# Optimization experiments

Hardware: AMD Instinct MI355X
Metric: run time of the kernel (lower is better)

Reference implementation:

```python
import jax, jax.numpy as jnp
import numpy as np

B = 128
D_IN = 1024
D_OUT = 512
N_PTS = 8192


def _fps(xyz, npoint):
    """Deterministic farthest_point_sample (initial farthest index = 0).
    xyz: [B, N, 3] -> idx [B, npoint]."""
    Bn, N, _ = xyz.shape
    bidx = jnp.arange(Bn)

    def step(carry, _):
        dist, far = carry
        centroid = xyz[bidx, far]                              # [B, 3]
        d = jnp.sum((xyz - centroid[:, None, :]) ** 2, -1)     # [B, N]
        dist = jnp.minimum(dist, d)
        return (dist, jnp.argmax(dist, -1)), far

    init = (jnp.full((Bn, N), 1e10, xyz.dtype), jnp.zeros((Bn,), jnp.int32))
    _, idxs = jax.lax.scan(step, init, None, length=npoint)    # [npoint, B]
    return idxs.T


def _proj(x, cw, cb, s, t, lw, lb):
    """Conv1d(k=1) -> eval BatchNorm (folded affine) -> ReLU -> Linear over length -> ReLU.
    x: [B, L, D_IN] -> [B, D_OUT, 32]."""
    h = jnp.einsum('bld,od->bol', x, cw) + cb[None, :, None]
    h = jax.nn.relu(h * s[None, :, None] + t[None, :, None])
    return jax.nn.relu(jnp.einsum('bol,sl->bos', h, lw) + lb)


def _pos_enc(xyz, w1, b1, s1, t1, w2, b2, s2, t2):
    """xyz: [B, n, 3] -> [B, n, D_OUT]. Two 1x1 convs with folded-affine BN + ReLU."""
    h = jnp.einsum('bnc,oc->bon', xyz, w1) + b1[None, :, None]
    h = jax.nn.relu(h * s1[None, :, None] + t1[None, :, None])
    h = jnp.einsum('bon,po->bpn', h, w2) + b2[None, :, None]
    h = jax.nn.relu(h * s2[None, :, None] + t2[None, :, None])
    return h.transpose(0, 2, 1)


def setup_inputs() -> dict:
    key = jax.random.key(0)
    ks = iter(jax.random.split(key, 64))

    def rn(shape, scale=0.05):
        return jax.random.normal(next(ks), shape, jnp.float32) * scale

    inp = {
        'rgb_feature': rn((B, 49, D_IN), 1.0),
        'depth_feature': rn((B, 49, D_IN), 1.0),
        'mmwave_feature': rn((B, 32, D_IN), 1.0),
        'lidar_feature': rn((B, 32, D_IN), 1.0),
        'lidar_points': rn((B, N_PTS, 3), 1.0),
    }
    for mod, L in (('rgb', 49), ('depth', 49), ('mmwave', 32), ('lidar', 32)):
        inp[f'{mod}_cw'] = rn((D_OUT, D_IN))
        inp[f'{mod}_cb'] = rn((D_OUT,))
        inp[f'{mod}_bns'] = jax.random.uniform(next(ks), (D_OUT,), jnp.float32, 0.5, 1.5)
        inp[f'{mod}_bnb'] = rn((D_OUT,))
        inp[f'{mod}_lw'] = rn((32, L))
        inp[f'{mod}_lb'] = rn((32,))
    inp['pe_w1'] = rn((128, 3), 0.5)
    inp['pe_b1'] = rn((128,))
    inp['pe_s1'] = jax.random.uniform(next(ks), (128,), jnp.float32, 0.5, 1.5)
    inp['pe_t1'] = rn((128,))
    inp['pe_w2'] = rn((D_OUT, 128))
    inp['pe_b2'] = rn((D_OUT,))
    inp['pe_s2'] = jax.random.uniform(next(ks), (D_OUT,), jnp.float32, 0.5, 1.5)
    inp['pe_t2'] = rn((D_OUT,))
    return inp


def reference(rgb_feature, depth_feature, mmwave_feature, lidar_feature, lidar_points,
              rgb_cw, rgb_cb, rgb_bns, rgb_bnb, rgb_lw, rgb_lb,
              depth_cw, depth_cb, depth_bns, depth_bnb, depth_lw, depth_lb,
              mmwave_cw, mmwave_cb, mmwave_bns, mmwave_bnb, mmwave_lw, mmwave_lb,
              lidar_cw, lidar_cb, lidar_bns, lidar_bnb, lidar_lw, lidar_lb,
              pe_w1, pe_b1, pe_s1, pe_t1, pe_w2, pe_b2, pe_s2, pe_t2):
    feats = [
        _proj(rgb_feature, rgb_cw, rgb_cb, rgb_bns, rgb_bnb, rgb_lw, rgb_lb),
        _proj(depth_feature, depth_cw, depth_cb, depth_bns, depth_bnb, depth_lw, depth_lb),
        _proj(mmwave_feature, mmwave_cw, mmwave_cb, mmwave_bns, mmwave_bnb, mmwave_lw, mmwave_lb),
        _proj(lidar_feature, lidar_cw, lidar_cb, lidar_bns, lidar_bnb, lidar_lw, lidar_lb),
    ]
    projected = jnp.concatenate(feats, axis=2).transpose(0, 2, 1)   # [B, 128, D_OUT]
    npoint = projected.shape[1]
    fps_idx = _fps(lidar_points, npoint)                            # [B, 128]
    new_xyz = jnp.take_along_axis(lidar_points, fps_idx[..., None], axis=1)  # [B, 128, 3]
    pos = _pos_enc(new_xyz, pe_w1, pe_b1, pe_s1, pe_t1, pe_w2, pe_b2, pe_s2, pe_t2)
    return projected + pos
```

## Files before the change

### kernel.cpp

```cpp
#include <hip/hip_runtime.h>
#include <hip/hip_bf16.h>

typedef __attribute__((ext_vector_type(8))) short bf16x8;
typedef __attribute__((ext_vector_type(4))) float f32x4;
typedef __attribute__((ext_vector_type(4))) float vf4;
typedef __attribute__((ext_vector_type(4))) short s16x4;
typedef __attribute__((ext_vector_type(2))) unsigned int u32x2;

__device__ __forceinline__ unsigned short f2bf(float f) {
  __hip_bfloat16 h = __float2bfloat16(f);
  union { __hip_bfloat16 h; unsigned short u; } cv; cv.h = h; return cv.u;
}

__device__ __forceinline__ u32x2 cvt4(vf4 v) {
  union { __hip_bfloat162 h; unsigned u; } a, b;
  a.h = __float22bfloat162_rn(make_float2(v[0], v[1]));
  b.h = __float22bfloat162_rn(make_float2(v[2], v[3]));
  u32x2 r; r[0] = a.u; r[1] = b.u; return r;
}

__device__ __forceinline__ void gemm_tile(const float* __restrict__ A,
                                          const float* __restrict__ W,
                                          const float* __restrict__ cbp,
                                          const float* __restrict__ scp,
                                          const float* __restrict__ shp,
                                          unsigned short* __restrict__ H,
                                          float* __restrict__ out,
                                          const int K, const int nk,
                                          const int mtile, const int ntile,
                                          unsigned short (&As)[128][64],
                                          unsigned short (&Bs)[128][64]) {
  const int t = threadIdx.x, lane = t & 63, wv = t >> 6;
  const int wr = wv >> 2, wc = wv & 3;
  const float* Ap = A + (size_t)(mtile * 128 + (t >> 4)) * K + ((t & 15) << 2);
  const float* Wp = W + (size_t)(ntile * 128 + (t >> 4)) * K + ((t & 15) << 2);
  const int sRow = t >> 4;
  const int sCol = (t & 15) << 2;

  f32x4 acc[4][2];
#pragma unroll
  for (int i = 0; i < 4; ++i)
#pragma unroll
    for (int j = 0; j < 2; ++j) acc[i][j] = (f32x4){0.f, 0.f, 0.f, 0.f};

  for (int ks = 0; ks < nk; ++ks) {
    __syncthreads();
#pragma unroll
    for (int p = 0; p < 4; ++p) {
      const vf4 av  = *(const vf4*)(Ap + (size_t)(p * 32) * K);
      const vf4 wvv = *(const vf4*)(Wp + (size_t)(p * 32) * K);
      *(u32x2*)&As[sRow + p * 32][sCol] = cvt4(av);
      *(u32x2*)&Bs[sRow + p * 32][sCol] = cvt4(wvv);
    }
    __syncthreads();
#pragma unroll
    for (int kk = 0; kk < 2; ++kk) {
      const int kb = (kk << 5) + ((lane >> 4) << 3);
      bf16x8 af[4], bfv[2];
#pragma unroll
      for (int i = 0; i < 4; ++i)
        af[i] = *(const bf16x8*)&As[wr * 64 + i * 16 + (lane & 15)][kb];
#pragma unroll
      for (int j = 0; j < 2; ++j)
        bfv[j] = *(const bf16x8*)&Bs[wc * 32 + j * 16 + (lane & 15)][kb];
#pragma unroll
      for (int i = 0; i < 4; ++i)
#pragma unroll
        for (int j = 0; j < 2; ++j)
          acc[i][j] = __builtin_amdgcn_mfma_f32_16x16x32_bf16(af[i], bfv[j], acc[i][j], 0, 0, 0);
    }
    Ap += 64; Wp += 64;
  }

  const int mbase = mtile * 128 + wr * 64;
  const int nbase = ntile * 128 + wc * 32;
#pragma unroll
  for (int j = 0; j < 2; ++j) {
    const int col = nbase + j * 16 + (lane & 15);
    const float cbv = cbp[col], scv = scp[col], shv = shp[col];
#pragma unroll
    for (int i = 0; i < 4; ++i) {
#pragma unroll
      for (int q = 0; q < 4; ++q) {
        const int row = mbase + i * 16 + ((lane >> 4) << 2) + q;
        float v = acc[i][j][q];
        v = fmaxf(fmaf(v + cbv, scv, shv), 0.f);
        if (H) H[(size_t)row * 512 + col] = f2bf(v);
        else   out[(size_t)row * 512 + col] = v;
      }
    }
  }
}

struct FArgs {
  const float* A[4]; const float* W[4];
  const float* cb[4]; const float* sc[4]; const float* sh[4];
  unsigned short* H[4];
  const float* pts; float* new_xyz;
};

__global__ __launch_bounds__(512) void fused_main(FArgs fa) {
  __shared__ __align__(16) unsigned short As[128][64];
  __shared__ __align__(16) unsigned short Bs[128][64];
  __shared__ unsigned long long red[2][8];
  __shared__ float redC[2][8][3];
  const int bid = blockIdx.x;

  if (bid < 128) {
    const int t = threadIdx.x, wv = t >> 6, lane = t & 63;
    const float* src = fa.pts + (size_t)bid * 8192 * 3;
    float px[16], py[16], pz[16], dist[16];
#pragma unroll
    for (int k = 0; k < 16; ++k) {
      const int p = t + (k << 9);
      px[k] = src[p * 3 + 0]; py[k] = src[p * 3 + 1]; pz[k] = src[p * 3 + 2];
      dist[k] = 1e10f;
    }
    float cx = src[0], cy = src[1], cz = src[2];
    for (int it = 0; it < 128; ++it) {
      if (t == 0) {
        float* o = fa.new_xyz + ((size_t)bid * 128 + it) * 3;
        o[0] = cx; o[1] = cy; o[2] = cz;
      }
      float bd = -1.f, bx = 0.f, by = 0.f, bz = 0.f; int bi = 0;
#pragma unroll
      for (int k = 0; k < 16; ++k) {
        const float dx = px[k] - cx, dy = py[k] - cy, dz = pz[k] - cz;
        const float d = __fadd_rn(__fadd_rn(__fmul_rn(dx, dx), __fmul_rn(dy, dy)),
                                  __fmul_rn(dz, dz));
        const float dk = fminf(dist[k], d);
        dist[k] = dk;
        if (dk > bd) { bd = dk; bi = t + (k << 9); bx = px[k]; by = py[k]; bz = pz[k]; }
      }
      const unsigned long long myKey =
          ((unsigned long long)__float_as_uint(bd) << 13) | (unsigned)(8191 - bi);
      unsigned long long key = myKey;
#pragma unroll
      for (int off = 32; off; off >>= 1) {
        const unsigned long long o = __shfl_xor(key, off);
        key = (o > key) ? o : key;
      }
      const int p = it & 1;
      if (lane == 0) red[p][wv] = key;
      if (myKey == key) {
        redC[p][wv][0] = bx; redC[p][wv][1] = by; redC[p][wv][2] = bz;
      }
      __syncthreads();
      unsigned long long m = red[p][0]; int w = 0;
#pragma unroll
      for (int i = 1; i < 8; ++i) {
        const unsigned long long v = red[p][i];
        if (v > m) { m = v; w = i; }
      }
      cx = redC[p][w][0]; cy = redC[p][w][1]; cz = redC[p][w][2];
    }
  } else {
    const int cb = bid - 128;
    int g, lid;
    if (cb < 196)      { g = 0; lid = cb; }
    else if (cb < 392) { g = 1; lid = cb - 196; }
    else if (cb < 520) { g = 2; lid = cb - 392; }
    else               { g = 3; lid = cb - 520; }
    gemm_tile(fa.A[g], fa.W[g], fa.cb[g], fa.sc[g], fa.sh[g], fa.H[g], nullptr,
              1024, 16, lid >> 2, lid & 3, As, Bs);
  }
}

__global__ __launch_bounds__(256) void posenc_h1(const float* __restrict__ nx,
                                                 const float* __restrict__ w1,
                                                 const float* __restrict__ b1,
                                                 const float* __restrict__ s1,
                                                 const float* __restrict__ t1,
                                                 float* __restrict__ H1) {
  const int gid = blockIdx.x * 256 + threadIdx.x;
  const int row = gid >> 7, j = gid & 127;
  const float x = nx[row * 3 + 0], y = nx[row * 3 + 1], z = nx[row * 3 + 2];
  float v = w1[j * 3 + 0] * x + w1[j * 3 + 1] * y + w1[j * 3 + 2] * z + b1[j];
  v = fmaxf(fmaf(v, s1[j], t1[j]), 0.f);
  H1[gid] = v;
}

struct PArgs {
  const float *A, *W, *cb, *sc, *sh;
  float* out;
};
__global__ __launch_bounds__(512) void gemm_pe(PArgs pa) {
  __shared__ __align__(16) unsigned short As[128][64];
  __shared__ __align__(16) unsigned short Bs[128][64];
  const int lid = blockIdx.x;
  gemm_tile(pa.A, pa.W, pa.cb, pa.sc, pa.sh, nullptr, pa.out,
            128, 2, lid >> 2, lid & 3, As, Bs);
}

struct MArgs {
  const unsigned short *H0, *H1, *H2, *H3;
  const float *lw0, *lw1, *lw2, *lw3;
  const float *lb0, *lb1, *lb2, *lb3;
  float* out;
};

__global__ __launch_bounds__(512) void mix_add(MArgs ma) {
  __shared__ float hs[49 * 512];
  __shared__ float lws[32 * 49];
  __shared__ float lbs[32];
  const int b = blockIdx.x >> 2, mod = blockIdx.x & 3, t = threadIdx.x;
  const unsigned short* H; const float* lw; const float* lb; int L;
  switch (mod) {
    case 0: H = ma.H0; lw = ma.lw0; lb = ma.lb0; L = 49; break;
    case 1: H = ma.H1; lw = ma.lw1; lb = ma.lb1; L = 49; break;
    case 2: H = ma.H2; lw = ma.lw2; lb = ma.lb2; L = 32; break;
    default:H = ma.H3; lw = ma.lw3; lb = ma.lb3; L = 32; break;
  }
  H += (size_t)b * L * 512;
  for (int i = t; i < L * 512; i += 512) hs[i] = __uint_as_float(((unsigned)H[i]) << 16);
  for (int i = t; i < 32 * L; i += 512) lws[i] = lw[i];
  if (t < 32) lbs[t] = lb[t];
  __syncthreads();
  float acc[32];
#pragma unroll
  for (int s = 0; s < 32; ++s) acc[s] = 0.f;
  for (int l = 0; l < L; ++l) {
    const float hv = hs[l * 512 + t];
#pragma unroll
    for (int s = 0; s < 32; ++s) acc[s] = fmaf(hv, lws[s * L + l], acc[s]);
  }
  float* O = ma.out + ((size_t)(b * 128 + mod * 32)) * 512 + t;
#pragma unroll
  for (int s = 0; s < 32; ++s) {
    O[(size_t)s * 512] += fmaxf(acc[s] + lbs[s], 0.f);
  }
}

extern "C" void kernel_launch(void* const* d_in, const int* in_sizes, int n_in,
                              void* d_out, int out_size, void* d_ws, size_t ws_size,
                              hipStream_t stream) {
  const float* rgb    = (const float*)d_in[0];
  const float* depth  = (const float*)d_in[1];
  const float* mmw    = (const float*)d_in[2];
  const float* lidf   = (const float*)d_in[3];
  const float* pts    = (const float*)d_in[4];

  const float* cw[4]  = { (const float*)d_in[5],  (const float*)d_in[11],
                          (const float*)d_in[17], (const float*)d_in[23] };
  const float* cb[4]  = { (const float*)d_in[6],  (const float*)d_in[12],
                          (const float*)d_in[18], (const float*)d_in[24] };
  const float* bns[4] = { (const float*)d_in[7],  (const float*)d_in[13],
                          (const float*)d_in[19], (const float*)d_in[25] };
  const float* bnb[4] = { (const float*)d_in[8],  (const float*)d_in[14],
                          (const float*)d_in[20], (const float*)d_in[26] };
  const float* lw[4]  = { (const float*)d_in[9],  (const float*)d_in[15],
                          (const float*)d_in[21], (const float*)d_in[27] };
  const float* lb[4]  = { (const float*)d_in[10], (const float*)d_in[16],
                          (const float*)d_in[22], (const float*)d_in[28] };

  const float* pe_w1 = (const float*)d_in[29];
  const float* pe_b1 = (const float*)d_in[30];
  const float* pe_s1 = (const float*)d_in[31];
  const float* pe_t1 = (const float*)d_in[32];
  const float* pe_w2 = (const float*)d_in[33];
  const float* pe_b2 = (const float*)d_in[34];
  const float* pe_s2 = (const float*)d_in[35];
  const float* pe_t2 = (const float*)d_in[36];

  char* ws = (char*)d_ws;
  float* new_xyz = (float*)ws;
  float* H1f     = (float*)(ws + 196608);
  unsigned short* h0 = (unsigned short*)(ws + 196608 + 8388608);
  unsigned short* h1 = h0 + (size_t)6272 * 512;
  unsigned short* h2 = h1 + (size_t)6272 * 512;
  unsigned short* h3 = h2 + (size_t)4096 * 512;
  float* out = (float*)d_out;

  FArgs fa;
  for (int i = 0; i < 4; ++i) {
    fa.A[i] = (i == 0) ? rgb : (i == 1) ? depth : (i == 2) ? mmw : lidf;
    fa.W[i] = cw[i]; fa.cb[i] = cb[i]; fa.sc[i] = bns[i]; fa.sh[i] = bnb[i];
  }
  fa.H[0] = h0; fa.H[1] = h1; fa.H[2] = h2; fa.H[3] = h3;
  fa.pts = pts; fa.new_xyz = new_xyz;
  fused_main<<<776, 512, 0, stream>>>(fa);

  posenc_h1<<<8192, 256, 0, stream>>>(new_xyz, pe_w1, pe_b1, pe_s1, pe_t1, H1f);

  PArgs pa;
  pa.A = H1f; pa.W = pe_w2; pa.cb = pe_b2; pa.sc = pe_s2; pa.sh = pe_t2;
  pa.out = out;
  gemm_pe<<<512, 512, 0, stream>>>(pa);

  MArgs ma;
  ma.H0 = h0; ma.H1 = h1; ma.H2 = h2; ma.H3 = h3;
  ma.lw0 = lw[0]; ma.lw1 = lw[1]; ma.lw2 = lw[2]; ma.lw3 = lw[3];
  ma.lb0 = lb[0]; ma.lb1 = lb[1]; ma.lb2 = lb[2]; ma.lb3 = lb[3];
  ma.out = out;
  mix_add<<<512, 512, 0, stream>>>(ma);
}
```

Before: 443.5 us.

## Fuse posenc first layer into PE GEMM, pad LDS, prioritize FPS waves

Computes the first positional-encoding layer (3→128 conv + BN + ReLU) on the fly while loading the A tile of the second-layer GEMM. This removes the posenc_h1 kernel and its 8 MB intermediate round trip through memory. It also pads the LDS tiles to 72 columns to cut bank conflicts, adds occupancy hints via launch_bounds(512,2), and raises scheduling priority for the FPS blocks. mix_add now stages bf16 in LDS with vector copies, converting to float per read. The trade-off is redundant first-layer arithmetic across N tiles and more LDS.

```diff
diff --git a/kernel.cpp b/kernel.cpp
--- a/kernel.cpp
+++ b/kernel.cpp
@@ -4,7 +4,6 @@
 typedef __attribute__((ext_vector_type(8))) short bf16x8;
 typedef __attribute__((ext_vector_type(4))) float f32x4;
 typedef __attribute__((ext_vector_type(4))) float vf4;
-typedef __attribute__((ext_vector_type(4))) short s16x4;
 typedef __attribute__((ext_vector_type(2))) unsigned int u32x2;
 
 __device__ __forceinline__ unsigned short f2bf(float f) {
@@ -19,17 +18,22 @@
   u32x2 r; r[0] = a.u; r[1] = b.u; return r;
 }
 
-__device__ __forceinline__ void gemm_tile(const float* __restrict__ A,
-                                          const float* __restrict__ W,
-                                          const float* __restrict__ cbp,
-                                          const float* __restrict__ scp,
-                                          const float* __restrict__ shp,
-                                          unsigned short* __restrict__ H,
-                                          float* __restrict__ out,
-                                          const int K, const int nk,
-                                          const int mtile, const int ntile,
-                                          unsigned short (&As)[128][64],
-                                          unsigned short (&Bs)[128][64]) {
+template <bool PE>
+__device__ __forceinline__ void gemm_tile_t(const float* __restrict__ A,
+                                            const float* __restrict__ W,
+                                            const float* __restrict__ cbp,
+                                            const float* __restrict__ scp,
+                                            const float* __restrict__ shp,
+                                            const float* __restrict__ w1,
+                                            const float* __restrict__ b1,
+                                            const float* __restrict__ s1,
+                                            const float* __restrict__ t1,
+                                            unsigned short* __restrict__ H,
+                                            float* __restrict__ out,
+                                            const int K, const int nk,
+                                            const int mtile, const int ntile,
+                                            unsigned short (&As)[128][72],
+                                            unsigned short (&Bs)[128][72]) {
   const int t = threadIdx.x, lane = t & 63, wv = t >> 6;
   const int wr = wv >> 2, wc = wv & 3;
   const float* Ap = A + (size_t)(mtile * 128 + (t >> 4)) * K + ((t & 15) << 2);
@@ -47,7 +51,19 @@
     __syncthreads();
 #pragma unroll
     for (int p = 0; p < 4; ++p) {
-      const vf4 av  = *(const vf4*)(Ap + (size_t)(p * 32) * K);
+      vf4 av;
+      if constexpr (PE) {
+        const int row = mtile * 128 + sRow + p * 32;
+        const float x = A[row * 3 + 0], y = A[row * 3 + 1], z = A[row * 3 + 2];
+#pragma unroll
+        for (int cc = 0; cc < 4; ++cc) {
+          const int j = ks * 64 + sCol + cc;
+          float v = w1[j * 3 + 0] * x + w1[j * 3 + 1] * y + w1[j * 3 + 2] * z + b1[j];
+          av[cc] = fmaxf(fmaf(v, s1[j], t1[j]), 0.f);
+        }
+      } else {
+        av = *(const vf4*)(Ap + (size_t)(p * 32) * K);
+      }
       const vf4 wvv = *(const vf4*)(Wp + (size_t)(p * 32) * K);
       *(u32x2*)&As[sRow + p * 32][sCol] = cvt4(av);
       *(u32x2*)&Bs[sRow + p * 32][sCol] = cvt4(wvv);
@@ -99,14 +115,15 @@
   const float* pts; float* new_xyz;
 };
 
-__global__ __launch_bounds__(512) void fused_main(FArgs fa) {
-  __shared__ __align__(16) unsigned short As[128][64];
-  __shared__ __align__(16) unsigned short Bs[128][64];
+__global__ __launch_bounds__(512, 2) void fused_main(FArgs fa) {
+  __shared__ __align__(16) unsigned short As[128][72];
+  __shared__ __align__(16) unsigned short Bs[128][72];
   __shared__ unsigned long long red[2][8];
   __shared__ float redC[2][8][3];
   const int bid = blockIdx.x;
 
   if (bid < 128) {
+    __builtin_amdgcn_s_setprio(3);
     const int t = threadIdx.x, wv = t >> 6, lane = t & 63;
     const float* src = fa.pts + (size_t)bid * 8192 * 3;
     float px[16], py[16], pz[16], dist[16];
@@ -161,35 +178,24 @@
     else if (cb < 392) { g = 1; lid = cb - 196; }
     else if (cb < 520) { g = 2; lid = cb - 392; }
     else               { g = 3; lid = cb - 520; }
-    gemm_tile(fa.A[g], fa.W[g], fa.cb[g], fa.sc[g], fa.sh[g], fa.H[g], nullptr,
-              1024, 16, lid >> 2, lid & 3, As, Bs);
-  }
-}
-
-__global__ __launch_bounds__(256) void posenc_h1(const float* __restrict__ nx,
-                                                 const float* __restrict__ w1,
-                                                 const float* __restrict__ b1,
-                                                 const float* __restrict__ s1,
-                                                 const float* __restrict__ t1,
-                                                 float* __restrict__ H1) {
-  const int gid = blockIdx.x * 256 + threadIdx.x;
-  const int row = gid >> 7, j = gid & 127;
-  const float x = nx[row * 3 + 0], y = nx[row * 3 + 1], z = nx[row * 3 + 2];
-  float v = w1[j * 3 + 0] * x + w1[j * 3 + 1] * y + w1[j * 3 + 2] * z + b1[j];
-  v = fmaxf(fmaf(v, s1[j], t1[j]), 0.f);
-  H1[gid] = v;
+    gemm_tile_t<false>(fa.A[g], fa.W[g], fa.cb[g], fa.sc[g], fa.sh[g],
+                       nullptr, nullptr, nullptr, nullptr,
+                       fa.H[g], nullptr, 1024, 16, lid >> 2, lid & 3, As, Bs);
+  }
 }
 
 struct PArgs {
-  const float *A, *W, *cb, *sc, *sh;
+  const float *xyz, *w1, *b1, *s1, *t1;
+  const float *W, *cb, *sc, *sh;
   float* out;
 };
-__global__ __launch_bounds__(512) void gemm_pe(PArgs pa) {
-  __shared__ __align__(16) unsigned short As[128][64];
-  __shared__ __align__(16) unsigned short Bs[128][64];
+__global__ __launch_bounds__(512, 2) void gemm_pe(PArgs pa) {
+  __shared__ __align__(16) unsigned short As[128][72];
+  __shared__ __align__(16) unsigned short Bs[128][72];
   const int lid = blockIdx.x;
-  gemm_tile(pa.A, pa.W, pa.cb, pa.sc, pa.sh, nullptr, pa.out,
-            128, 2, lid >> 2, lid & 3, As, Bs);
+  gemm_tile_t<true>(pa.xyz, pa.W, pa.cb, pa.sc, pa.sh,
+                    pa.w1, pa.b1, pa.s1, pa.t1,
+                    nullptr, pa.out, 128, 2, lid >> 2, lid & 3, As, Bs);
 }
 
 struct MArgs {
@@ -200,7 +206,7 @@
 };
 
 __global__ __launch_bounds__(512) void mix_add(MArgs ma) {
-  __shared__ float hs[49 * 512];
+  __shared__ unsigned short hsb[49 * 512];
   __shared__ float lws[32 * 49];
   __shared__ float lbs[32];
   const int b = blockIdx.x >> 2, mod = blockIdx.x & 3, t = threadIdx.x;
@@ -212,7 +218,9 @@
     default:H = ma.H3; lw = ma.lw3; lb = ma.lb3; L = 32; break;
   }
   H += (size_t)b * L * 512;
-  for (int i = t; i < L * 512; i += 512) hs[i] = __uint_as_float(((unsigned)H[i]) << 16);
+  const int nv = (L * 512) >> 3;
+  for (int i = t; i < nv; i += 512)
+    *(bf16x8*)&hsb[i << 3] = *(const bf16x8*)&H[i << 3];
   for (int i = t; i < 32 * L; i += 512) lws[i] = lw[i];
   if (t < 32) lbs[t] = lb[t];
   __syncthreads();
@@ -220,7 +228,7 @@
 #pragma unroll
   for (int s = 0; s < 32; ++s) acc[s] = 0.f;
   for (int l = 0; l < L; ++l) {
-    const float hv = hs[l * 512 + t];
+    const float hv = __uint_as_float(((unsigned)hsb[l * 512 + t]) << 16);
 #pragma unroll
     for (int s = 0; s < 32; ++s) acc[s] = fmaf(hv, lws[s * L + l], acc[s]);
   }
@@ -264,8 +272,7 @@
 
   char* ws = (char*)d_ws;
   float* new_xyz = (float*)ws;
-  float* H1f     = (float*)(ws + 196608);
-  unsigned short* h0 = (unsigned short*)(ws + 196608 + 8388608);
+  unsigned short* h0 = (unsigned short*)(ws + 196608);
   unsigned short* h1 = h0 + (size_t)6272 * 512;
   unsigned short* h2 = h1 + (size_t)6272 * 512;
   unsigned short* h3 = h2 + (size_t)4096 * 512;
@@ -280,10 +287,9 @@
   fa.pts = pts; fa.new_xyz = new_xyz;
   fused_main<<<776, 512, 0, stream>>>(fa);
 
-  posenc_h1<<<8192, 256, 0, stream>>>(new_xyz, pe_w1, pe_b1, pe_s1, pe_t1, H1f);
-
   PArgs pa;
-  pa.A = H1f; pa.W = pe_w2; pa.cb = pe_b2; pa.sc = pe_s2; pa.sh = pe_t2;
+  pa.xyz = new_xyz; pa.w1 = pe_w1; pa.b1 = pe_b1; pa.s1 = pe_s1; pa.t1 = pe_t1;
+  pa.W = pe_w2; pa.cb = pe_b2; pa.sc = pe_s2; pa.sh = pe_t2;
   pa.out = out;
   gemm_pe<<<512, 512, 0, stream>>>(pa);
 
```

Result: faster. 419.9 us (-5.3%).
